# Kernel tuning notes

Measured on AMD Instinct MI355X. Metric: run time of the kernel, lower is better.

## Reference

```python
import jax, jax.numpy as jnp
import numpy as np
from math import sqrt

NUM_HEADS = 16
DIM_MODEL = 1024


def setup_inputs() -> dict:
    key = jax.random.key(0)
    ks = jax.random.split(key, 12)
    B, S, D, M = 4, 1024, DIM_MODEL, 64
    bound = 1.0 / sqrt(D)
    def lin_w(k):
        return jax.random.uniform(k, (D, D), jnp.float32, -bound, bound)
    def lin_b(k):
        return jax.random.uniform(k, (D,), jnp.float32, -bound, bound)
    return {
        "query": jax.random.normal(ks[0], (B, S, D), jnp.float32),
        "key": jax.random.normal(ks[1], (B, S, D), jnp.float32),
        "value": jax.random.normal(ks[2], (B, S, D), jnp.float32),
        "mask": jax.random.randint(ks[3], (1, B, S, M), 0, 2).astype(jnp.float32),
        "Wq": lin_w(ks[4]), "bq": lin_b(ks[5]),
        "Wk": lin_w(ks[6]), "bk": lin_b(ks[7]),
        "Wv": lin_w(ks[8]), "bv": lin_b(ks[9]),
        "Wo": lin_w(ks[10]),
    }


def reference(query, key, value, mask, Wq, bq, Wk, bk, Wv, bv, Wo):
    B, S, D = query.shape
    H = NUM_HEADS
    d = D // H
    # projections + head split, permute(2,0,1,3) -> [H,B,S,d]
    q = (query @ Wq.T + bq).reshape(B, S, H, d).transpose(2, 0, 1, 3)
    k = (key @ Wk.T + bk).reshape(B, S, H, d).transpose(2, 0, 1, 3)
    v = (value @ Wv.T + bv).reshape(B, S, H, d).transpose(2, 0, 1, 3)
    attn = jnp.einsum("hbqd,hbkd->hbqk", q, k) / sqrt(d)  # [H,B,S,S]
    # custom mask: mask.repeat(H,1,1,1) then mask @ mask^T / sqrt(m).
    # Identical per-head, so compute once on [B,S,m] and broadcast over H.
    m2d = mask[0]  # [B,S,m]
    mm = jnp.einsum("bqm,bkm->bqk", m2d, m2d) / sqrt(m2d.shape[-1])
    attn = jnp.where(mm[None] == 0, jnp.float32(-1e9), attn)
    w = jax.nn.softmax(attn, axis=-1)  # dropout is identity in eval mode
    x = jnp.einsum("hbqk,hbkd->hbqd", w, v)  # [H,B,S,d]
    # torch: permute(1,2,0,3) -> [B,S,H,d]; transpose(1,2) -> [B,H,S,d];
    # contiguous().view(B,-1,H*d) -- row-major reshape (mixes head/seq layout, replicated faithfully)
    x = jnp.transpose(x, (1, 0, 2, 3))  # [B,H,S,d]
    x = x.reshape(B, -1, H * d)
    return x @ Wo.T
```

## Files before the change

kernel.cpp:

```cpp
#include <hip/hip_runtime.h>

typedef unsigned int u32;
typedef unsigned short u16;
typedef unsigned long long u64;
typedef __attribute__((ext_vector_type(8))) short s16x8;
typedef __attribute__((ext_vector_type(8))) __bf16 bf16x8;
typedef __attribute__((ext_vector_type(4))) float f32x4;

#define WSMB (1ull << 20)

static __device__ __forceinline__ u16 f2bf(float f) {
  u32 u = __builtin_bit_cast(u32, f);
  return (u16)((u + 0x7fffu + ((u >> 16) & 1u)) >> 16);
}

static __device__ __forceinline__ u32 pkbf(float lo, float hi) {
  u32 r;
  asm("v_cvt_pk_bf16_f32 %0, %1, %2" : "=v"(r) : "v"(lo), "v"(hi));
  return r;
}

static __device__ __forceinline__ f32x4 mfma16x16(s16x8 a, s16x8 b, f32x4 c) {
  return __builtin_amdgcn_mfma_f32_16x16x32_bf16(
      __builtin_bit_cast(bf16x8, a), __builtin_bit_cast(bf16x8, b), c, 0, 0, 0);
}

#define GLOAD_LDS16(g, l)                                                      \
  __builtin_amdgcn_global_load_lds(                                            \
      (const __attribute__((address_space(1))) u32*)(const void*)(g),          \
      (__attribute__((address_space(3))) u32*)(void*)(l), 16, 0, 0)

__global__ __launch_bounds__(256) void k_cvt3(const float* __restrict__ a,
                                              const float* __restrict__ b,
                                              const float* __restrict__ c,
                                              u16* __restrict__ oa,
                                              u16* __restrict__ ob,
                                              u16* __restrict__ oc) {
  const float* s;
  u16* d;
  if (blockIdx.y == 0) { s = a; d = oa; }
  else if (blockIdx.y == 1) { s = b; d = ob; }
  else { s = c; d = oc; }
  int i = (blockIdx.x * 256 + threadIdx.x) * 4;
  float4 v = *(const float4*)(s + i);
  u64 p = (u64)f2bf(v.x) | ((u64)f2bf(v.y) << 16) | ((u64)f2bf(v.z) << 32) |
          ((u64)f2bf(v.w) << 48);
  *(u64*)(d + i) = p;
}

__global__ __launch_bounds__(256) void k_cvt4(const float* __restrict__ a,
                                              const float* __restrict__ b,
                                              const float* __restrict__ c,
                                              const float* __restrict__ e,
                                              u16* __restrict__ oa,
                                              u16* __restrict__ ob,
                                              u16* __restrict__ oc,
                                              u16* __restrict__ oe) {
  const float* s;
  u16* d;
  if (blockIdx.y == 0) { s = a; d = oa; }
  else if (blockIdx.y == 1) { s = b; d = ob; }
  else if (blockIdx.y == 2) { s = c; d = oc; }
  else { s = e; d = oe; }
  int i = (blockIdx.x * 256 + threadIdx.x) * 4;
  float4 v = *(const float4*)(s + i);
  u64 p = (u64)f2bf(v.x) | ((u64)f2bf(v.y) << 16) | ((u64)f2bf(v.z) << 32) |
          ((u64)f2bf(v.w) << 48);
  *(u64*)(d + i) = p;
}

__global__ __launch_bounds__(256) void k_bits(const float* __restrict__ mask,
                                              u64* __restrict__ bits) {
  int w = threadIdx.x >> 6, l = threadIdx.x & 63;
  int r = blockIdx.x * 4 + w;
  float v = mask[(size_t)r * 64 + l];
  u64 bl = __ballot(v != 0.0f);
  if (l == 0) bits[r] = bl;
}

__global__ __launch_bounds__(256) void k_mm(const u64* __restrict__ bits,
                                            u64* __restrict__ MB) {
  int wv = threadIdx.x >> 6, l = threadIdx.x & 63;
  int qg = blockIdx.x * 4 + wv;
  u64 bq = bits[qg];
  const u64* bb = bits + (qg & ~1023);
  u64* out = MB + (size_t)qg * 16;
  for (int kt = 0; kt < 16; kt++) {
    u64 bk = bb[kt * 64 + l];
    u64 m = __ballot((bq & bk) != 0ull);
    if (l == 0) out[kt] = m;
  }
}

static __device__ __forceinline__ void gemm_core(const u16* __restrict__ A,
                                                 const u16* __restrict__ Bw,
                                                 f32x4 (&acc)[4][4]) {
  __shared__ __attribute__((aligned(16))) u16 As[2][4096];
  __shared__ __attribute__((aligned(16))) u16 Bs[2][4096];
  const int t = threadIdx.x;
  const int l = t & 63, w = t >> 6, lr = l & 15, lk = l >> 4;
  const int amr = (w & 1) * 64, bnr = (w >> 1) * 64;
  const int c0 = t, c1 = t + 256;
  const int r0 = c0 >> 2, r1 = c1 >> 2;
  const int sw0 = ((c0 & 3) * 8) ^ ((r0 & 6) << 2);
  const int sw1 = ((c1 & 3) * 8) ^ ((r1 & 6) << 2);
  const u16* Ag0 = A + (size_t)r0 * 1024 + sw0;
  const u16* Ag1 = A + (size_t)r1 * 1024 + sw1;
  const u16* Bg0 = Bw + (size_t)r0 * 1024 + sw0;
  const u16* Bg1 = Bw + (size_t)r1 * 1024 + sw1;
  const int aswz = (lk * 16) ^ ((lr & 6) << 3);

  GLOAD_LDS16(Ag0, &As[0][c0 * 8]);
  GLOAD_LDS16(Ag1, &As[0][c1 * 8]);
  GLOAD_LDS16(Bg0, &Bs[0][c0 * 8]);
  GLOAD_LDS16(Bg1, &Bs[0][c1 * 8]);

  int cur = 0;
  for (int kt = 0; kt < 1024; kt += 32) {
    __syncthreads();
    if (kt < 992) {
      const int nxt = cur ^ 1;
      GLOAD_LDS16(Ag0 + kt + 32, &As[nxt][c0 * 8]);
      GLOAD_LDS16(Ag1 + kt + 32, &As[nxt][c1 * 8]);
      GLOAD_LDS16(Bg0 + kt + 32, &Bs[nxt][c0 * 8]);
      GLOAD_LDS16(Bg1 + kt + 32, &Bs[nxt][c1 * 8]);
    }
    const char* Ac = (const char*)As[cur];
    const char* Bc = (const char*)Bs[cur];
    s16x8 af[4], bf[4];
#pragma unroll
    for (int i = 0; i < 4; i++)
      af[i] = *(const s16x8*)(Ac + (amr + i * 16 + lr) * 64 + aswz);
#pragma unroll
    for (int j = 0; j < 4; j++)
      bf[j] = *(const s16x8*)(Bc + (bnr + j * 16 + lr) * 64 + aswz);
    __builtin_amdgcn_s_setprio(1);
#pragma unroll
    for (int i = 0; i < 4; i++)
#pragma unroll
      for (int j = 0; j < 4; j++)
        acc[i][j] = mfma16x16(af[i], bf[j], acc[i][j]);
    __builtin_amdgcn_s_setprio(0);
    cur ^= 1;
  }
}

__global__ __launch_bounds__(256) void k_qkv(
    const u16* __restrict__ Xq, const u16* __restrict__ Xk,
    const u16* __restrict__ Xv, const u16* __restrict__ Wqb,
    const u16* __restrict__ Wkb, const u16* __restrict__ Wvb,
    const float* __restrict__ bq, const float* __restrict__ bk,
    const float* __restrict__ bv, u16* __restrict__ Qo, u16* __restrict__ Ko,
    u16* __restrict__ V4) {
  const int bid0 = blockIdx.x;
  const int bid = (bid0 & 7) * 96 + (bid0 >> 3);
  const int proj = bid >> 8;
  const int rem = bid & 255;
  const int st = rem >> 3, dt = rem & 7;
  const u16* Xp = proj == 0 ? Xq : (proj == 1 ? Xk : Xv);
  const u16* Wp = proj == 0 ? Wqb : (proj == 1 ? Wkb : Wvb);
  const float* bias = proj == 0 ? bq : (proj == 1 ? bk : bv);
  const int t = threadIdx.x;
  const int l = t & 63, w = t >> 6, lr = l & 15, lk = l >> 4;
  const int amr = (w & 1) * 64, bnr = (w >> 1) * 64;
  f32x4 acc[4][4] = {};
  if (proj < 2) {
    gemm_core(Wp + (size_t)dt * 131072, Xp + (size_t)st * 131072, acc);
    u16* O = proj ? Ko : Qo;
#pragma unroll
    for (int i = 0; i < 4; i++) {
      const int d0 = dt * 128 + amr + i * 16 + lk * 4;
      const int h = d0 >> 6, dd0 = d0 & 63;
      const float4 b4 = *(const float4*)(bias + d0);
#pragma unroll
      for (int j = 0; j < 4; j++) {
        const int s = st * 128 + bnr + j * 16 + lr;
        const int b_ = s >> 10, si = s & 1023;
        u32 e0 = pkbf(acc[i][j][0] + b4.x, acc[i][j][1] + b4.y);
        u32 e1 = pkbf(acc[i][j][2] + b4.z, acc[i][j][3] + b4.w);
        *(u64*)(O + ((size_t)((b_ * 16 + h) * 1024 + si)) * 64 + dd0) =
            (u64)e0 | ((u64)e1 << 32);
      }
    }
  } else {
    gemm_core(Xp + (size_t)st * 131072, Wp + (size_t)dt * 131072, acc);
#pragma unroll
    for (int i = 0; i < 4; i++) {
      const int s0 = st * 128 + amr + i * 16 + lk * 4;
      const int b_ = s0 >> 10, si = s0 & 1023;
      const int sblk = si >> 3, soff = si & 7;
#pragma unroll
      for (int j = 0; j < 4; j++) {
        const int d = dt * 128 + bnr + j * 16 + lr;
        const int h = d >> 6, dd = d & 63;
        const float bb = bias[d];
        u32 e0 = pkbf(acc[i][j][0] + bb, acc[i][j][1] + bb);
        u32 e1 = pkbf(acc[i][j][2] + bb, acc[i][j][3] + bb);
        *(u64*)(V4 + (size_t)(b_ * 16 + h) * 65536 +
                (size_t)(sblk * 64 + dd) * 8 + soff) =
            (u64)e0 | ((u64)e1 << 32);
      }
    }
  }
}

__global__ __launch_bounds__(256) void k_oproj(const u16* __restrict__ Xb,
                                               const u16* __restrict__ Wob,
                                               float* __restrict__ Out) {
  const int bid0 = blockIdx.x;
  const int bid = (bid0 & 7) * 32 + (bid0 >> 3);
  const int mb = bid >> 3, nb = bid & 7;
  f32x4 acc[4][4] = {};
  gemm_core(Xb + (size_t)mb * 131072, Wob + (size_t)nb * 131072, acc);
  const int t = threadIdx.x;
  const int l = t & 63, w = t >> 6, lr = l & 15, lk = l >> 4;
  const int amr = (w & 1) * 64, bnr = (w >> 1) * 64;
#pragma unroll
  for (int i = 0; i < 4; i++)
#pragma unroll
    for (int j = 0; j < 4; j++)
#pragma unroll
      for (int r = 0; r < 4; r++) {
        const int m = mb * 128 + amr + i * 16 + lk * 4 + r;
        const int n = nb * 128 + bnr + j * 16 + lr;
        Out[(size_t)m * 1024 + n] = acc[i][j][r];
      }
}

__global__ __launch_bounds__(256, 4) void k_attn(const u16* __restrict__ Qb,
                                                 const u16* __restrict__ Kb,
                                                 const u16* __restrict__ V4,
                                                 const u64* __restrict__ MB,
                                                 u16* __restrict__ xbuf) {
  __shared__ __attribute__((aligned(16))) u16 Ks[2][4096];
  __shared__ __attribute__((aligned(16))) u16 Vs[2][4096];
  __shared__ __attribute__((aligned(16))) u16 Ps[4][1024];
  const int t = threadIdx.x, l = t & 63, w = t >> 6, lr = l & 15, lk = l >> 4;
  const int bid = (blockIdx.x & 7) * 128 + (blockIdx.x >> 3);
  const int qt = bid & 15, hb = bid >> 4;
  const int h = hb >> 2, b = hb & 3;
  const int s0 = qt * 64;
  const u16* Qhb = Qb + (size_t)(b * 16 + h) * 65536;
  const u16* Khb = Kb + (size_t)(b * 16 + h) * 65536;
  const u16* Vhb = V4 + (size_t)(b * 16 + h) * 65536;
  const int q = s0 + w * 16 + lr;
  const u64* MBq = MB + ((size_t)b * 1024 + q) * 16;

  s16x8 qf0 = *(const s16x8*)(Qhb + (size_t)q * 64 + lk * 8);
  s16x8 qf1 = *(const s16x8*)(Qhb + (size_t)q * 64 + 32 + lk * 8);

  f32x4 xa[4] = {};
  float m_ = -__builtin_inff(), ls = 0.f;

  const int ca = t, cb_ = t + 256;
  const int rA = ca >> 3, colA = (ca & 7) * 16;
  const int rB = cb_ >> 3, colB = (cb_ & 7) * 16;
  const int sA = colA ^ ((rA & 7) << 4);
  const int sB = colB ^ ((rB & 7) << 4);
  const u16* KgA = Khb + (size_t)rA * 64 + (sA >> 1);
  const u16* KgB = Khb + (size_t)rB * 64 + (sB >> 1);
  const u16* VgA = Vhb + (size_t)(sA >> 4) * 512 + rA * 8;
  const u16* VgB = Vhb + (size_t)(sB >> 4) * 512 + rB * 8;

  GLOAD_LDS16(KgA, &Ks[0][ca * 8]);
  GLOAD_LDS16(KgB, &Ks[0][cb_ * 8]);
  GLOAD_LDS16(VgA, &Vs[0][ca * 8]);
  GLOAD_LDS16(VgB, &Vs[0][cb_ * 8]);

  int cur = 0;
  for (int kt = 0; kt < 16; kt++) {
    __syncthreads();
    if (kt < 15) {
      const int nxt = cur ^ 1;
      GLOAD_LDS16(KgA + (kt + 1) * 4096, &Ks[nxt][ca * 8]);
      GLOAD_LDS16(KgB + (kt + 1) * 4096, &Ks[nxt][cb_ * 8]);
      GLOAD_LDS16(VgA + (kt + 1) * 4096, &Vs[nxt][ca * 8]);
      GLOAD_LDS16(VgB + (kt + 1) * 4096, &Vs[nxt][cb_ * 8]);
    }
    const u16* Kc = Ks[cur];
    const u16* Vc = Vs[cur];
    const int kb = kt * 64;

    u64 mw = MBq[kt];
    u32 mlo = (u32)(mw >> (lk * 4));
    u32 mhi = (u32)(mw >> (lk * 4 + 32));
    float p[4][4];
#pragma unroll
    for (int nb = 0; nb < 4; nb++) {
      const int krow = nb * 16 + lr;
      const int sw = (krow & 7) << 4;
      s16x8 k0 = *(const s16x8*)((const char*)Kc + krow * 128 + ((lk * 16) ^ sw));
      s16x8 k1 =
          *(const s16x8*)((const char*)Kc + krow * 128 + ((64 + lk * 16) ^ sw));
      f32x4 z = {};
      __builtin_amdgcn_s_setprio(1);
      z = mfma16x16(k0, qf0, z);
      z = mfma16x16(k1, qf1, z);
      __builtin_amdgcn_s_setprio(0);
#pragma unroll
      for (int r = 0; r < 4; r++) p[nb][r] = z[r] * 0.125f;
    }
    (void)kb;

    float tm = fmaxf(fmaxf(p[0][0], p[0][1]), fmaxf(p[0][2], p[0][3]));
#pragma unroll
    for (int nb = 1; nb < 4; nb++)
      tm = fmaxf(tm,
                 fmaxf(fmaxf(p[nb][0], p[nb][1]), fmaxf(p[nb][2], p[nb][3])));
    tm = fmaxf(tm, __shfl_xor(tm, 16));
    tm = fmaxf(tm, __shfl_xor(tm, 32));
    const float mn = fmaxf(m_, tm);
    const float scl = __expf(m_ - mn);
    m_ = mn;
    float ts = 0.f;
#pragma unroll
    for (int nb = 0; nb < 4; nb++) {
      const u32 mword = (nb & 2) ? mhi : mlo;
#pragma unroll
      for (int r = 0; r < 4; r++) {
        float e = __expf(p[nb][r] - mn);
        e = ((mword >> ((nb & 1) * 16 + r)) & 1u) ? e : 0.f;
        p[nb][r] = e;
        ts += e;
      }
    }
    ts += __shfl_xor(ts, 16);
    ts += __shfl_xor(ts, 32);
    ls = ls * scl + ts;
#pragma unroll
    for (int nd = 0; nd < 4; nd++) xa[nd] *= scl;

    char* Pw = (char*)&Ps[w][0];
#pragma unroll
    for (int nb = 0; nb < 4; nb++) {
      u32 w0 = pkbf(p[nb][0], p[nb][1]);
      u32 w1 = pkbf(p[nb][2], p[nb][3]);
      *(u64*)(Pw + lr * 128 + ((nb * 32 + lk * 8) ^ ((lr & 7) << 4))) =
          (u64)w0 | ((u64)w1 << 32);
    }
    const int sw2 = (lr & 7) << 4;
    s16x8 pb0 = *(const s16x8*)(Pw + lr * 128 + ((lk * 16) ^ sw2));
    s16x8 pb1 = *(const s16x8*)(Pw + lr * 128 + ((64 + lk * 16) ^ sw2));

    __builtin_amdgcn_s_setprio(1);
#pragma unroll
    for (int nd = 0; nd < 4; nd++) {
      const int vrow = nd * 16 + lr;
      const int vsw = (vrow & 7) << 4;
      s16x8 v0 = *(const s16x8*)((const char*)Vc + vrow * 128 + ((lk * 16) ^ vsw));
      s16x8 v1 =
          *(const s16x8*)((const char*)Vc + vrow * 128 + ((64 + lk * 16) ^ vsw));
      xa[nd] = mfma16x16(v0, pb0, xa[nd]);
      xa[nd] = mfma16x16(v1, pb1, xa[nd]);
    }
    __builtin_amdgcn_s_setprio(0);
    cur ^= 1;
  }

  const float inv = 1.0f / ls;
  const size_t rowb = (size_t)b * 1048576 + (size_t)(h * 64 + (q >> 4)) * 1024 +
                      (size_t)(q & 15) * 64;
#pragma unroll
  for (int nd = 0; nd < 4; nd++) {
    u32 e0 = pkbf(xa[nd][0] * inv, xa[nd][1] * inv);
    u32 e1 = pkbf(xa[nd][2] * inv, xa[nd][3] * inv);
    *(u64*)(xbuf + rowb + nd * 16 + lk * 4) = (u64)e0 | ((u64)e1 << 32);
  }
}

extern "C" void kernel_launch(void* const* d_in, const int* in_sizes, int n_in,
                              void* d_out, int out_size, void* d_ws,
                              size_t ws_size, hipStream_t stream) {
  const float* query = (const float*)d_in[0];
  const float* key_ = (const float*)d_in[1];
  const float* value = (const float*)d_in[2];
  const float* mask = (const float*)d_in[3];
  const float* bq = (const float*)d_in[5];
  const float* bk = (const float*)d_in[7];
  const float* bv = (const float*)d_in[9];
  const float* Wq = (const float*)d_in[4];
  const float* Wk = (const float*)d_in[6];
  const float* Wv = (const float*)d_in[8];
  const float* Wo = (const float*)d_in[10];

  char* ws = (char*)d_ws;
  u16* Xq = (u16*)(ws + 0 * WSMB);
  u16* Xk = (u16*)(ws + 8 * WSMB);
  u16* Xv = (u16*)(ws + 16 * WSMB);
  u16* Wqb = (u16*)(ws + 24 * WSMB);
  u16* Wkb = (u16*)(ws + 26 * WSMB);
  u16* Wvb = (u16*)(ws + 28 * WSMB);
  u16* Wob = (u16*)(ws + 30 * WSMB);
  u16* Qb = (u16*)(ws + 32 * WSMB);
  u16* Kb = (u16*)(ws + 40 * WSMB);
  u16* V4 = (u16*)(ws + 48 * WSMB);
  u64* bits = (u64*)(ws + 56 * WSMB);
  u64* MBm = (u64*)(ws + 8 * WSMB);
  u16* xbuf = Xq;

  k_cvt3<<<dim3(4096, 3), 256, 0, stream>>>(query, key_, value, Xq, Xk, Xv);
  k_cvt4<<<dim3(1024, 4), 256, 0, stream>>>(Wq, Wk, Wv, Wo, Wqb, Wkb, Wvb, Wob);
  k_bits<<<1024, 256, 0, stream>>>(mask, bits);
  k_qkv<<<768, 256, 0, stream>>>(Xq, Xk, Xv, Wqb, Wkb, Wvb, bq, bk, bv, Qb, Kb,
                                 V4);
  k_mm<<<1024, 256, 0, stream>>>(bits, MBm);
  k_attn<<<1024, 256, 0, stream>>>(Qb, Kb, V4, MBm, xbuf);
  k_oproj<<<256, 256, 0, stream>>>(xbuf, Wob, (float*)d_out);
}
```

Measured before the change: 129.1 us.

## Process two query tiles per wave, fold softmax scale into Q, lazy rescale

Each wave now handles 32 query rows (two 16-row groups) that share every K and V fragment read from LDS, halving the grid to 512 blocks and doubling K/V reuse. The softmax scale 1/sqrt(d)·log2(e) is folded into the Q projection epilogue so scores feed v_exp_f32 (base-2 exp) directly without a per-score multiply. The running-max rescale is skipped unless the new tile max exceeds the old one by more than 8, which avoids exp and accumulator multiplies on most tiles. The mask word for the next key tile is also prefetched. In exchange, register pressure rises (launch bounds drop to 2 blocks) and fewer, larger blocks may lower occupancy.

```diff
diff --git a/kernel.cpp b/kernel.cpp
--- a/kernel.cpp
+++ b/kernel.cpp
@@ -8,6 +8,7 @@
 typedef __attribute__((ext_vector_type(4))) float f32x4;
 
 #define WSMB (1ull << 20)
+#define QSC 0.18033688011112042f
 
 static __device__ __forceinline__ u16 f2bf(float f) {
   u32 u = __builtin_bit_cast(u32, f);
@@ -17,6 +18,12 @@
 static __device__ __forceinline__ u32 pkbf(float lo, float hi) {
   u32 r;
   asm("v_cvt_pk_bf16_f32 %0, %1, %2" : "=v"(r) : "v"(lo), "v"(hi));
+  return r;
+}
+
+static __device__ __forceinline__ float ex2(float x) {
+  float r;
+  asm("v_exp_f32 %0, %1" : "=v"(r) : "v"(x));
   return r;
 }
 
@@ -165,6 +172,7 @@
   const int amr = (w & 1) * 64, bnr = (w >> 1) * 64;
   f32x4 acc[4][4] = {};
   if (proj < 2) {
+    const float sc = proj == 0 ? QSC : 1.0f;
     gemm_core(Wp + (size_t)dt * 131072, Xp + (size_t)st * 131072, acc);
     u16* O = proj ? Ko : Qo;
 #pragma unroll
@@ -176,8 +184,8 @@
       for (int j = 0; j < 4; j++) {
         const int s = st * 128 + bnr + j * 16 + lr;
         const int b_ = s >> 10, si = s & 1023;
-        u32 e0 = pkbf(acc[i][j][0] + b4.x, acc[i][j][1] + b4.y);
-        u32 e1 = pkbf(acc[i][j][2] + b4.z, acc[i][j][3] + b4.w);
+        u32 e0 = pkbf((acc[i][j][0] + b4.x) * sc, (acc[i][j][1] + b4.y) * sc);
+        u32 e1 = pkbf((acc[i][j][2] + b4.z) * sc, (acc[i][j][3] + b4.w) * sc);
         *(u64*)(O + ((size_t)((b_ * 16 + h) * 1024 + si)) * 64 + dd0) =
             (u64)e0 | ((u64)e1 << 32);
       }
@@ -227,30 +235,70 @@
       }
 }
 
-__global__ __launch_bounds__(256, 4) void k_attn(const u16* __restrict__ Qb,
+static __device__ __forceinline__ void softmax_g(float (&p)[4][4], u64 mw,
+                                                 int lk, float& m_, float& ls,
+                                                 f32x4 (&xa)[4]) {
+  const u32 mlo = (u32)(mw >> (lk * 4));
+  const u32 mhi = (u32)(mw >> (lk * 4 + 32));
+  float tm = fmaxf(fmaxf(p[0][0], p[0][1]), fmaxf(p[0][2], p[0][3]));
+#pragma unroll
+  for (int nb = 1; nb < 4; nb++)
+    tm = fmaxf(tm, fmaxf(fmaxf(p[nb][0], p[nb][1]), fmaxf(p[nb][2], p[nb][3])));
+  tm = fmaxf(tm, __shfl_xor(tm, 16));
+  tm = fmaxf(tm, __shfl_xor(tm, 32));
+  if (!__all(tm <= m_ + 8.0f)) {
+    const float mn = fmaxf(m_, tm);
+    const float scl = ex2(m_ - mn);
+    m_ = mn;
+    ls *= scl;
+#pragma unroll
+    for (int nd = 0; nd < 4; nd++) xa[nd] *= scl;
+  }
+  float ts = 0.f;
+#pragma unroll
+  for (int nb = 0; nb < 4; nb++) {
+    const u32 mword = (nb & 2) ? mhi : mlo;
+#pragma unroll
+    for (int r = 0; r < 4; r++) {
+      float e = ex2(p[nb][r] - m_);
+      e = ((mword >> ((nb & 1) * 16 + r)) & 1u) ? e : 0.f;
+      p[nb][r] = e;
+      ts += e;
+    }
+  }
+  ts += __shfl_xor(ts, 16);
+  ts += __shfl_xor(ts, 32);
+  ls += ts;
+}
+
+__global__ __launch_bounds__(256, 2) void k_attn(const u16* __restrict__ Qb,
                                                  const u16* __restrict__ Kb,
                                                  const u16* __restrict__ V4,
                                                  const u64* __restrict__ MB,
                                                  u16* __restrict__ xbuf) {
   __shared__ __attribute__((aligned(16))) u16 Ks[2][4096];
   __shared__ __attribute__((aligned(16))) u16 Vs[2][4096];
-  __shared__ __attribute__((aligned(16))) u16 Ps[4][1024];
+  __shared__ __attribute__((aligned(16))) u16 Ps[4][2048];
   const int t = threadIdx.x, l = t & 63, w = t >> 6, lr = l & 15, lk = l >> 4;
-  const int bid = (blockIdx.x & 7) * 128 + (blockIdx.x >> 3);
-  const int qt = bid & 15, hb = bid >> 4;
+  const int bid = (blockIdx.x & 7) * 64 + (blockIdx.x >> 3);
+  const int qt = bid & 7, hb = bid >> 3;
   const int h = hb >> 2, b = hb & 3;
-  const int s0 = qt * 64;
+  const int s0 = qt * 128;
   const u16* Qhb = Qb + (size_t)(b * 16 + h) * 65536;
   const u16* Khb = Kb + (size_t)(b * 16 + h) * 65536;
   const u16* Vhb = V4 + (size_t)(b * 16 + h) * 65536;
-  const int q = s0 + w * 16 + lr;
-  const u64* MBq = MB + ((size_t)b * 1024 + q) * 16;
-
-  s16x8 qf0 = *(const s16x8*)(Qhb + (size_t)q * 64 + lk * 8);
-  s16x8 qf1 = *(const s16x8*)(Qhb + (size_t)q * 64 + 32 + lk * 8);
-
-  f32x4 xa[4] = {};
-  float m_ = -__builtin_inff(), ls = 0.f;
+  const int qA = s0 + w * 32 + lr, qB = qA + 16;
+  const u64* MBA = MB + ((size_t)b * 1024 + qA) * 16;
+  const u64* MBB = MB + ((size_t)b * 1024 + qB) * 16;
+
+  s16x8 qfA0 = *(const s16x8*)(Qhb + (size_t)qA * 64 + lk * 8);
+  s16x8 qfA1 = *(const s16x8*)(Qhb + (size_t)qA * 64 + 32 + lk * 8);
+  s16x8 qfB0 = *(const s16x8*)(Qhb + (size_t)qB * 64 + lk * 8);
+  s16x8 qfB1 = *(const s16x8*)(Qhb + (size_t)qB * 64 + 32 + lk * 8);
+
+  f32x4 xaA[4] = {}, xaB[4] = {};
+  float mA = -__builtin_inff(), lsA = 0.f;
+  float mB = -__builtin_inff(), lsB = 0.f;
 
   const int ca = t, cb_ = t + 256;
   const int rA = ca >> 3, colA = (ca & 7) * 16;
@@ -266,6 +314,7 @@
   GLOAD_LDS16(KgB, &Ks[0][cb_ * 8]);
   GLOAD_LDS16(VgA, &Vs[0][ca * 8]);
   GLOAD_LDS16(VgB, &Vs[0][cb_ * 8]);
+  u64 mwA = MBA[0], mwB = MBB[0];
 
   int cur = 0;
   for (int kt = 0; kt < 16; kt++) {
@@ -277,14 +326,12 @@
       GLOAD_LDS16(VgA + (kt + 1) * 4096, &Vs[nxt][ca * 8]);
       GLOAD_LDS16(VgB + (kt + 1) * 4096, &Vs[nxt][cb_ * 8]);
     }
+    const int ktn = (kt + 1) & 15;
+    const u64 nwA = MBA[ktn], nwB = MBB[ktn];
     const u16* Kc = Ks[cur];
     const u16* Vc = Vs[cur];
-    const int kb = kt * 64;
-
-    u64 mw = MBq[kt];
-    u32 mlo = (u32)(mw >> (lk * 4));
-    u32 mhi = (u32)(mw >> (lk * 4 + 32));
-    float p[4][4];
+
+    float pA[4][4], pB[4][4];
 #pragma unroll
     for (int nb = 0; nb < 4; nb++) {
       const int krow = nb * 16 + lr;
@@ -292,55 +339,39 @@
       s16x8 k0 = *(const s16x8*)((const char*)Kc + krow * 128 + ((lk * 16) ^ sw));
       s16x8 k1 =
           *(const s16x8*)((const char*)Kc + krow * 128 + ((64 + lk * 16) ^ sw));
-      f32x4 z = {};
+      f32x4 zA = {}, zB = {};
       __builtin_amdgcn_s_setprio(1);
-      z = mfma16x16(k0, qf0, z);
-      z = mfma16x16(k1, qf1, z);
+      zA = mfma16x16(k0, qfA0, zA);
+      zA = mfma16x16(k1, qfA1, zA);
+      zB = mfma16x16(k0, qfB0, zB);
+      zB = mfma16x16(k1, qfB1, zB);
       __builtin_amdgcn_s_setprio(0);
 #pragma unroll
-      for (int r = 0; r < 4; r++) p[nb][r] = z[r] * 0.125f;
-    }
-    (void)kb;
-
-    float tm = fmaxf(fmaxf(p[0][0], p[0][1]), fmaxf(p[0][2], p[0][3]));
-#pragma unroll
-    for (int nb = 1; nb < 4; nb++)
-      tm = fmaxf(tm,
-                 fmaxf(fmaxf(p[nb][0], p[nb][1]), fmaxf(p[nb][2], p[nb][3])));
-    tm = fmaxf(tm, __shfl_xor(tm, 16));
-    tm = fmaxf(tm, __shfl_xor(tm, 32));
-    const float mn = fmaxf(m_, tm);
-    const float scl = __expf(m_ - mn);
-    m_ = mn;
-    float ts = 0.f;
+      for (int r = 0; r < 4; r++) {
+        pA[nb][r] = zA[r];
+        pB[nb][r] = zB[r];
+      }
+    }
+
+    softmax_g(pA, mwA, lk, mA, lsA, xaA);
+    softmax_g(pB, mwB, lk, mB, lsB, xaB);
+
+    char* Pw = (char*)&Ps[w][0];
 #pragma unroll
     for (int nb = 0; nb < 4; nb++) {
-      const u32 mword = (nb & 2) ? mhi : mlo;
-#pragma unroll
-      for (int r = 0; r < 4; r++) {
-        float e = __expf(p[nb][r] - mn);
-        e = ((mword >> ((nb & 1) * 16 + r)) & 1u) ? e : 0.f;
-        p[nb][r] = e;
-        ts += e;
-      }
-    }
-    ts += __shfl_xor(ts, 16);
-    ts += __shfl_xor(ts, 32);
-    ls = ls * scl + ts;
-#pragma unroll
-    for (int nd = 0; nd < 4; nd++) xa[nd] *= scl;
-
-    char* Pw = (char*)&Ps[w][0];
-#pragma unroll
-    for (int nb = 0; nb < 4; nb++) {
-      u32 w0 = pkbf(p[nb][0], p[nb][1]);
-      u32 w1 = pkbf(p[nb][2], p[nb][3]);
-      *(u64*)(Pw + lr * 128 + ((nb * 32 + lk * 8) ^ ((lr & 7) << 4))) =
-          (u64)w0 | ((u64)w1 << 32);
+      const int co = (nb * 32 + lk * 8) ^ ((lr & 7) << 4);
+      u32 a0 = pkbf(pA[nb][0], pA[nb][1]);
+      u32 a1 = pkbf(pA[nb][2], pA[nb][3]);
+      *(u64*)(Pw + lr * 128 + co) = (u64)a0 | ((u64)a1 << 32);
+      u32 b0 = pkbf(pB[nb][0], pB[nb][1]);
+      u32 b1 = pkbf(pB[nb][2], pB[nb][3]);
+      *(u64*)(Pw + (16 + lr) * 128 + co) = (u64)b0 | ((u64)b1 << 32);
     }
     const int sw2 = (lr & 7) << 4;
-    s16x8 pb0 = *(const s16x8*)(Pw + lr * 128 + ((lk * 16) ^ sw2));
-    s16x8 pb1 = *(const s16x8*)(Pw + lr * 128 + ((64 + lk * 16) ^ sw2));
+    s16x8 pa0 = *(const s16x8*)(Pw + lr * 128 + ((lk * 16) ^ sw2));
+    s16x8 pa1 = *(const s16x8*)(Pw + lr * 128 + ((64 + lk * 16) ^ sw2));
+    s16x8 pb0 = *(const s16x8*)(Pw + (16 + lr) * 128 + ((lk * 16) ^ sw2));
+    s16x8 pb1 = *(const s16x8*)(Pw + (16 + lr) * 128 + ((64 + lk * 16) ^ sw2));
 
     __builtin_amdgcn_s_setprio(1);
 #pragma unroll
@@ -350,21 +381,30 @@
       s16x8 v0 = *(const s16x8*)((const char*)Vc + vrow * 128 + ((lk * 16) ^ vsw));
       s16x8 v1 =
           *(const s16x8*)((const char*)Vc + vrow * 128 + ((64 + lk * 16) ^ vsw));
-      xa[nd] = mfma16x16(v0, pb0, xa[nd]);
-      xa[nd] = mfma16x16(v1, pb1, xa[nd]);
+      xaA[nd] = mfma16x16(v0, pa0, xaA[nd]);
+      xaA[nd] = mfma16x16(v1, pa1, xaA[nd]);
+      xaB[nd] = mfma16x16(v0, pb0, xaB[nd]);
+      xaB[nd] = mfma16x16(v1, pb1, xaB[nd]);
     }
     __builtin_amdgcn_s_setprio(0);
+    mwA = nwA;
+    mwB = nwB;
     cur ^= 1;
   }
 
-  const float inv = 1.0f / ls;
-  const size_t rowb = (size_t)b * 1048576 + (size_t)(h * 64 + (q >> 4)) * 1024 +
-                      (size_t)(q & 15) * 64;
+  const float invA = 1.0f / lsA, invB = 1.0f / lsB;
+  const size_t rbA = (size_t)b * 1048576 + (size_t)(h * 64 + (qA >> 4)) * 1024 +
+                     (size_t)(qA & 15) * 64;
+  const size_t rbB = (size_t)b * 1048576 + (size_t)(h * 64 + (qB >> 4)) * 1024 +
+                     (size_t)(qB & 15) * 64;
 #pragma unroll
   for (int nd = 0; nd < 4; nd++) {
-    u32 e0 = pkbf(xa[nd][0] * inv, xa[nd][1] * inv);
-    u32 e1 = pkbf(xa[nd][2] * inv, xa[nd][3] * inv);
-    *(u64*)(xbuf + rowb + nd * 16 + lk * 4) = (u64)e0 | ((u64)e1 << 32);
+    u32 a0 = pkbf(xaA[nd][0] * invA, xaA[nd][1] * invA);
+    u32 a1 = pkbf(xaA[nd][2] * invA, xaA[nd][3] * invA);
+    *(u64*)(xbuf + rbA + nd * 16 + lk * 4) = (u64)a0 | ((u64)a1 << 32);
+    u32 b0 = pkbf(xaB[nd][0] * invB, xaB[nd][1] * invB);
+    u32 b1 = pkbf(xaB[nd][2] * invB, xaB[nd][3] * invB);
+    *(u64*)(xbuf + rbB + nd * 16 + lk * 4) = (u64)b0 | ((u64)b1 << 32);
   }
 }
 
@@ -404,6 +444,6 @@
   k_qkv<<<768, 256, 0, stream>>>(Xq, Xk, Xv, Wqb, Wkb, Wvb, bq, bk, bv, Qb, Kb,
                                  V4);
   k_mm<<<1024, 256, 0, stream>>>(bits, MBm);
-  k_attn<<<1024, 256, 0, stream>>>(Qb, Kb, V4, MBm, xbuf);
+  k_attn<<<512, 256, 0, stream>>>(Qb, Kb, V4, MBm, xbuf);
   k_oproj<<<256, 256, 0, stream>>>(xbuf, Wob, (float*)d_out);
 }
```

New measurement: 127.8 us. Within noise of the previous version (-1.1%).

## Rewrite attention with 32x32 MFMA, register-resident P, and folded exp2 scaling

Applied to the files above, without the earlier changes.

The attention kernel now uses 32x32x16 bf16 MFMAs with 128-query tiles per block, which halves the grid and doubles the K/V reuse per block. The P matrix is kept in registers and repacked with permlane32 swaps instead of a round trip through LDS. Softmax uses raw v_exp_f32 with the 1/sqrt(d)*log2e scale folded into the Q projection. The running max is rescaled only when it increases, and masking is skipped when a whole wave's mask word is all ones. Trade-offs are higher register pressure (launch bounds lowered to 3) and fewer blocks available to fill the GPU.

```diff
diff --git a/kernel.cpp b/kernel.cpp
--- a/kernel.cpp
+++ b/kernel.cpp
@@ -6,8 +6,11 @@
 typedef __attribute__((ext_vector_type(8))) short s16x8;
 typedef __attribute__((ext_vector_type(8))) __bf16 bf16x8;
 typedef __attribute__((ext_vector_type(4))) float f32x4;
+typedef __attribute__((ext_vector_type(16))) float f32x16;
+typedef __attribute__((ext_vector_type(4))) u32 u32x4;
 
 #define WSMB (1ull << 20)
+#define QSC 0.18033688011112042f
 
 static __device__ __forceinline__ u16 f2bf(float f) {
   u32 u = __builtin_bit_cast(u32, f);
@@ -20,8 +23,19 @@
   return r;
 }
 
+static __device__ __forceinline__ float ex2(float x) {
+  float r;
+  asm("v_exp_f32 %0, %1" : "=v"(r) : "v"(x));
+  return r;
+}
+
 static __device__ __forceinline__ f32x4 mfma16x16(s16x8 a, s16x8 b, f32x4 c) {
   return __builtin_amdgcn_mfma_f32_16x16x32_bf16(
+      __builtin_bit_cast(bf16x8, a), __builtin_bit_cast(bf16x8, b), c, 0, 0, 0);
+}
+
+static __device__ __forceinline__ f32x16 mfma32x32(s16x8 a, s16x8 b, f32x16 c) {
+  return __builtin_amdgcn_mfma_f32_32x32x16_bf16(
       __builtin_bit_cast(bf16x8, a), __builtin_bit_cast(bf16x8, b), c, 0, 0, 0);
 }
 
@@ -165,6 +179,7 @@
   const int amr = (w & 1) * 64, bnr = (w >> 1) * 64;
   f32x4 acc[4][4] = {};
   if (proj < 2) {
+    const float sc = proj == 0 ? QSC : 1.0f;
     gemm_core(Wp + (size_t)dt * 131072, Xp + (size_t)st * 131072, acc);
     u16* O = proj ? Ko : Qo;
 #pragma unroll
@@ -176,8 +191,8 @@
       for (int j = 0; j < 4; j++) {
         const int s = st * 128 + bnr + j * 16 + lr;
         const int b_ = s >> 10, si = s & 1023;
-        u32 e0 = pkbf(acc[i][j][0] + b4.x, acc[i][j][1] + b4.y);
-        u32 e1 = pkbf(acc[i][j][2] + b4.z, acc[i][j][3] + b4.w);
+        u32 e0 = pkbf((acc[i][j][0] + b4.x) * sc, (acc[i][j][1] + b4.y) * sc);
+        u32 e1 = pkbf((acc[i][j][2] + b4.z) * sc, (acc[i][j][3] + b4.w) * sc);
         *(u64*)(O + ((size_t)((b_ * 16 + h) * 1024 + si)) * 64 + dd0) =
             (u64)e0 | ((u64)e1 << 32);
       }
@@ -227,30 +242,32 @@
       }
 }
 
-__global__ __launch_bounds__(256, 4) void k_attn(const u16* __restrict__ Qb,
+__global__ __launch_bounds__(256, 3) void k_attn(const u16* __restrict__ Qb,
                                                  const u16* __restrict__ Kb,
                                                  const u16* __restrict__ V4,
                                                  const u64* __restrict__ MB,
                                                  u16* __restrict__ xbuf) {
   __shared__ __attribute__((aligned(16))) u16 Ks[2][4096];
   __shared__ __attribute__((aligned(16))) u16 Vs[2][4096];
-  __shared__ __attribute__((aligned(16))) u16 Ps[4][1024];
-  const int t = threadIdx.x, l = t & 63, w = t >> 6, lr = l & 15, lk = l >> 4;
-  const int bid = (blockIdx.x & 7) * 128 + (blockIdx.x >> 3);
-  const int qt = bid & 15, hb = bid >> 4;
+  const int t = threadIdx.x, l = t & 63, w = t >> 6;
+  const int q5 = l & 31, hi = l >> 5;
+  const int bid = (blockIdx.x & 7) * 64 + (blockIdx.x >> 3);
+  const int qt = bid & 7, hb = bid >> 3;
   const int h = hb >> 2, b = hb & 3;
-  const int s0 = qt * 64;
+  const int s0 = qt * 128;
   const u16* Qhb = Qb + (size_t)(b * 16 + h) * 65536;
   const u16* Khb = Kb + (size_t)(b * 16 + h) * 65536;
   const u16* Vhb = V4 + (size_t)(b * 16 + h) * 65536;
-  const int q = s0 + w * 16 + lr;
+  const int q = s0 + w * 32 + q5;
   const u64* MBq = MB + ((size_t)b * 1024 + q) * 16;
 
-  s16x8 qf0 = *(const s16x8*)(Qhb + (size_t)q * 64 + lk * 8);
-  s16x8 qf1 = *(const s16x8*)(Qhb + (size_t)q * 64 + 32 + lk * 8);
-
-  f32x4 xa[4] = {};
-  float m_ = -__builtin_inff(), ls = 0.f;
+  s16x8 qf[4];
+#pragma unroll
+  for (int ds = 0; ds < 4; ds++)
+    qf[ds] = *(const s16x8*)(Qhb + (size_t)q * 64 + ds * 16 + hi * 8);
+
+  f32x16 xa0 = {}, xa1 = {};
+  float ls = 0.f, m_ = -__builtin_inff();
 
   const int ca = t, cb_ = t + 256;
   const int rA = ca >> 3, colA = (ca & 7) * 16;
@@ -262,10 +279,13 @@
   const u16* VgA = Vhb + (size_t)(sA >> 4) * 512 + rA * 8;
   const u16* VgB = Vhb + (size_t)(sB >> 4) * 512 + rB * 8;
 
+  const int rbase = q5 * 128 + ((hi * 16) ^ ((q5 & 7) << 4));
+
   GLOAD_LDS16(KgA, &Ks[0][ca * 8]);
   GLOAD_LDS16(KgB, &Ks[0][cb_ * 8]);
   GLOAD_LDS16(VgA, &Vs[0][ca * 8]);
   GLOAD_LDS16(VgB, &Vs[0][cb_ * 8]);
+  u64 mw = MBq[0];
 
   int cur = 0;
   for (int kt = 0; kt < 16; kt++) {
@@ -277,94 +297,101 @@
       GLOAD_LDS16(VgA + (kt + 1) * 4096, &Vs[nxt][ca * 8]);
       GLOAD_LDS16(VgB + (kt + 1) * 4096, &Vs[nxt][cb_ * 8]);
     }
-    const u16* Kc = Ks[cur];
-    const u16* Vc = Vs[cur];
-    const int kb = kt * 64;
-
-    u64 mw = MBq[kt];
-    u32 mlo = (u32)(mw >> (lk * 4));
-    u32 mhi = (u32)(mw >> (lk * 4 + 32));
-    float p[4][4];
-#pragma unroll
-    for (int nb = 0; nb < 4; nb++) {
-      const int krow = nb * 16 + lr;
-      const int sw = (krow & 7) << 4;
-      s16x8 k0 = *(const s16x8*)((const char*)Kc + krow * 128 + ((lk * 16) ^ sw));
-      s16x8 k1 =
-          *(const s16x8*)((const char*)Kc + krow * 128 + ((64 + lk * 16) ^ sw));
-      f32x4 z = {};
+    const u64 nw = MBq[(kt + 1) & 15];
+    const char* Kc = (const char*)Ks[cur];
+    const char* Vc = (const char*)Vs[cur];
+
+    f32x16 z0 = {}, z1 = {};
+#pragma unroll
+    for (int ds = 0; ds < 4; ds++) {
+      s16x8 k0 = *(const s16x8*)(Kc + (rbase ^ (ds * 32)));
+      s16x8 k1 = *(const s16x8*)(Kc + 4096 + (rbase ^ (ds * 32)));
       __builtin_amdgcn_s_setprio(1);
-      z = mfma16x16(k0, qf0, z);
-      z = mfma16x16(k1, qf1, z);
+      z0 = mfma32x32(k0, qf[ds], z0);
+      z1 = mfma32x32(k1, qf[ds], z1);
       __builtin_amdgcn_s_setprio(0);
-#pragma unroll
-      for (int r = 0; r < 4; r++) p[nb][r] = z[r] * 0.125f;
-    }
-    (void)kb;
-
-    float tm = fmaxf(fmaxf(p[0][0], p[0][1]), fmaxf(p[0][2], p[0][3]));
-#pragma unroll
-    for (int nb = 1; nb < 4; nb++)
-      tm = fmaxf(tm,
-                 fmaxf(fmaxf(p[nb][0], p[nb][1]), fmaxf(p[nb][2], p[nb][3])));
-    tm = fmaxf(tm, __shfl_xor(tm, 16));
+    }
+
+    float tmx[16];
+#pragma unroll
+    for (int r = 0; r < 16; r++) tmx[r] = fmaxf(z0[r], z1[r]);
+#pragma unroll
+    for (int st_ = 8; st_ >= 1; st_ >>= 1)
+#pragma unroll
+      for (int r = 0; r < 8; r++)
+        if (r < st_) tmx[r] = fmaxf(tmx[r], tmx[r + st_]);
+    float tm = tmx[0];
     tm = fmaxf(tm, __shfl_xor(tm, 32));
-    const float mn = fmaxf(m_, tm);
-    const float scl = __expf(m_ - mn);
-    m_ = mn;
+    if (tm > m_) {
+      const float scl = ex2(m_ - tm);
+      m_ = tm;
+      ls *= scl;
+      xa0 *= scl;
+      xa1 *= scl;
+    }
+
+    float e0[16], e1[16];
+#pragma unroll
+    for (int r = 0; r < 16; r++) e0[r] = ex2(z0[r] - m_);
+#pragma unroll
+    for (int r = 0; r < 16; r++) e1[r] = ex2(z1[r] - m_);
+    if (!__all(mw == ~0ull)) {
+      const u32 mh0 = (u32)(mw >> (hi * 4));
+      const u32 mh1 = (u32)(mw >> (hi * 4 + 32));
+#pragma unroll
+      for (int r = 0; r < 16; r++) {
+        const int bp = 8 * (r >> 2) + (r & 3);
+        e0[r] = ((mh0 >> bp) & 1u) ? e0[r] : 0.f;
+        e1[r] = ((mh1 >> bp) & 1u) ? e1[r] : 0.f;
+      }
+    }
     float ts = 0.f;
 #pragma unroll
-    for (int nb = 0; nb < 4; nb++) {
-      const u32 mword = (nb & 2) ? mhi : mlo;
-#pragma unroll
-      for (int r = 0; r < 4; r++) {
-        float e = __expf(p[nb][r] - mn);
-        e = ((mword >> ((nb & 1) * 16 + r)) & 1u) ? e : 0.f;
-        p[nb][r] = e;
-        ts += e;
-      }
-    }
-    ts += __shfl_xor(ts, 16);
-    ts += __shfl_xor(ts, 32);
-    ls = ls * scl + ts;
-#pragma unroll
-    for (int nd = 0; nd < 4; nd++) xa[nd] *= scl;
-
-    char* Pw = (char*)&Ps[w][0];
-#pragma unroll
-    for (int nb = 0; nb < 4; nb++) {
-      u32 w0 = pkbf(p[nb][0], p[nb][1]);
-      u32 w1 = pkbf(p[nb][2], p[nb][3]);
-      *(u64*)(Pw + lr * 128 + ((nb * 32 + lk * 8) ^ ((lr & 7) << 4))) =
-          (u64)w0 | ((u64)w1 << 32);
-    }
-    const int sw2 = (lr & 7) << 4;
-    s16x8 pb0 = *(const s16x8*)(Pw + lr * 128 + ((lk * 16) ^ sw2));
-    s16x8 pb1 = *(const s16x8*)(Pw + lr * 128 + ((64 + lk * 16) ^ sw2));
-
-    __builtin_amdgcn_s_setprio(1);
-#pragma unroll
-    for (int nd = 0; nd < 4; nd++) {
-      const int vrow = nd * 16 + lr;
-      const int vsw = (vrow & 7) << 4;
-      s16x8 v0 = *(const s16x8*)((const char*)Vc + vrow * 128 + ((lk * 16) ^ vsw));
-      s16x8 v1 =
-          *(const s16x8*)((const char*)Vc + vrow * 128 + ((64 + lk * 16) ^ vsw));
-      xa[nd] = mfma16x16(v0, pb0, xa[nd]);
-      xa[nd] = mfma16x16(v1, pb1, xa[nd]);
-    }
-    __builtin_amdgcn_s_setprio(0);
+    for (int r = 0; r < 16; r++) ts += e0[r] + e1[r];
+    ls += ts;
+
+    u32 P0[2][4], P1[2][4];
+#pragma unroll
+    for (int qi = 0; qi < 4; qi++) {
+      P0[0][qi] = pkbf(e0[4 * qi], e0[4 * qi + 1]);
+      P1[0][qi] = pkbf(e0[4 * qi + 2], e0[4 * qi + 3]);
+      P0[1][qi] = pkbf(e1[4 * qi], e1[4 * qi + 1]);
+      P1[1][qi] = pkbf(e1[4 * qi + 2], e1[4 * qi + 3]);
+    }
+
+#pragma unroll
+    for (int ks = 0; ks < 4; ks++) {
+      const int kb = ks >> 1, qi0 = (ks & 1) * 2, qi1 = qi0 + 1;
+      u32 w0 = P0[kb][qi0], w2 = P0[kb][qi1];
+      u32 w1 = P1[kb][qi0], w3 = P1[kb][qi1];
+      asm("v_permlane32_swap_b32 %0, %1" : "+v"(w0), "+v"(w2));
+      asm("v_permlane32_swap_b32 %0, %1" : "+v"(w1), "+v"(w3));
+      u32x4 fv;
+      fv[0] = w0; fv[1] = w1; fv[2] = w2; fv[3] = w3;
+      const s16x8 pb = __builtin_bit_cast(s16x8, fv);
+      s16x8 v0 = *(const s16x8*)(Vc + (rbase ^ (ks * 32)));
+      s16x8 v1 = *(const s16x8*)(Vc + 4096 + (rbase ^ (ks * 32)));
+      __builtin_amdgcn_s_setprio(1);
+      xa0 = mfma32x32(v0, pb, xa0);
+      xa1 = mfma32x32(v1, pb, xa1);
+      __builtin_amdgcn_s_setprio(0);
+    }
+    mw = nw;
     cur ^= 1;
   }
 
+  ls += __shfl_xor(ls, 32);
   const float inv = 1.0f / ls;
   const size_t rowb = (size_t)b * 1048576 + (size_t)(h * 64 + (q >> 4)) * 1024 +
                       (size_t)(q & 15) * 64;
 #pragma unroll
-  for (int nd = 0; nd < 4; nd++) {
-    u32 e0 = pkbf(xa[nd][0] * inv, xa[nd][1] * inv);
-    u32 e1 = pkbf(xa[nd][2] * inv, xa[nd][3] * inv);
-    *(u64*)(xbuf + rowb + nd * 16 + lk * 4) = (u64)e0 | ((u64)e1 << 32);
+  for (int qi = 0; qi < 4; qi++) {
+    u32 a0 = pkbf(xa0[4 * qi] * inv, xa0[4 * qi + 1] * inv);
+    u32 a1 = pkbf(xa0[4 * qi + 2] * inv, xa0[4 * qi + 3] * inv);
+    *(u64*)(xbuf + rowb + 8 * qi + 4 * hi) = (u64)a0 | ((u64)a1 << 32);
+    u32 b0 = pkbf(xa1[4 * qi] * inv, xa1[4 * qi + 1] * inv);
+    u32 b1 = pkbf(xa1[4 * qi + 2] * inv, xa1[4 * qi + 3] * inv);
+    *(u64*)(xbuf + rowb + 32 + 8 * qi + 4 * hi) = (u64)b0 | ((u64)b1 << 32);
   }
 }
 
@@ -404,6 +431,6 @@
   k_qkv<<<768, 256, 0, stream>>>(Xq, Xk, Xv, Wqb, Wkb, Wvb, bq, bk, bv, Qb, Kb,
                                  V4);
   k_mm<<<1024, 256, 0, stream>>>(bits, MBm);
-  k_attn<<<1024, 256, 0, stream>>>(Qb, Kb, V4, MBm, xbuf);
+  k_attn<<<512, 256, 0, stream>>>(Qb, Kb, V4, MBm, xbuf);
   k_oproj<<<256, 256, 0, stream>>>(xbuf, Wob, (float*)d_out);
 }
```

Result: faster. 119.0 us (-7.8%).
